# Optimization experiments

Hardware: AMD Instinct MI355X
Metric: run time of the kernel (lower is better)

Reference implementation:

```python
import jax, jax.numpy as jnp
import numpy as np

ALPHA = 1.702
LIMIT = 7.0


def setup_inputs() -> dict:
    key = jax.random.key(0)
    ks = jax.random.split(key, 7)
    B, S, H, D, E, TOPK = 2, 2048, 2048, 2048, 8, 4
    T = B * S
    hidden_states = jax.random.normal(ks[0], (B, S, H), dtype=jnp.float32)
    gate_up_proj = jax.random.normal(ks[1], (E, H, 2 * D), dtype=jnp.float32) * 0.02
    gate_up_proj_bias = jax.random.normal(ks[2], (E, 2 * D), dtype=jnp.float32) * 0.02
    down_proj = jax.random.normal(ks[3], (E, D, H), dtype=jnp.float32) * 0.02
    down_proj_bias = jax.random.normal(ks[4], (E, H), dtype=jnp.float32) * 0.02
    rw = jax.random.uniform(ks[5], (T, E), dtype=jnp.float32)
    routing_weights = rw / jnp.sum(rw, axis=-1, keepdims=True)
    router_indices = jax.random.randint(ks[6], (T, TOPK), 0, E, dtype=jnp.int64)
    return {
        "hidden_states": hidden_states,
        "gate_up_proj": gate_up_proj,
        "gate_up_proj_bias": gate_up_proj_bias,
        "down_proj": down_proj,
        "down_proj_bias": down_proj_bias,
        "routing_weights": routing_weights,
        "router_indices": router_indices,
    }


def geglu(gate_up):
    # interleaved layout: gate = [..., 0::2], up = [..., 1::2]
    gate = gate_up[..., 0::2]
    up = gate_up[..., 1::2]
    gate = jnp.minimum(gate, LIMIT)
    up = jnp.clip(up, -LIMIT, LIMIT)
    glu = gate * jax.nn.sigmoid(gate * ALPHA)
    return (up + 1.0) * glu


def reference(hidden_states, gate_up_proj, gate_up_proj_bias, down_proj,
              down_proj_bias, routing_weights, router_indices):
    B, S, H = hidden_states.shape
    x = hidden_states.reshape(-1, H)  # [T, H]
    # per-expert batched GEMM: [E, T, 2D]
    gate_up = jnp.einsum('th,ehd->etd', x, gate_up_proj) + gate_up_proj_bias[:, None, :]
    act = geglu(gate_up)  # [E, T, D]
    out = jnp.einsum('etd,edh->eth', act, down_proj) + down_proj_bias[:, None, :]
    # weight by router probs and sum over experts
    out = out * routing_weights.T[:, :, None]  # [E, T, H]
    out = jnp.sum(out, axis=0)
    return out.reshape(B, S, H)
```

## Files before the change

kernel.cpp:

```cpp
#include <hip/hip_runtime.h>
#include <hip/hip_bf16.h>

#define ALPHA 1.702f
#define GLIMIT 7.0f

typedef __attribute__((ext_vector_type(4))) float f32x4;
typedef __attribute__((ext_vector_type(8))) __bf16 bf16x8;
typedef __attribute__((ext_vector_type(8))) short short8;

typedef __attribute__((address_space(3))) unsigned int as3_uint;
typedef const __attribute__((address_space(1))) unsigned int as1_uint;

__device__ __forceinline__ void async_copy16(void* lds, const void* g) {
    __builtin_amdgcn_global_load_lds((as1_uint*)g, (as3_uint*)lds, 16, 0, 0);
}

__device__ __forceinline__ short f2bf(float f) {
    unsigned u = __float_as_uint(f);
    unsigned r = (u + 0x7fffu + ((u >> 16) & 1u)) >> 16;
    return (short)r;
}

__global__ void cvt_bf16_kernel(const float* __restrict__ src,
                                short* __restrict__ dst, int n4) {
    int i = blockIdx.x * blockDim.x + threadIdx.x;
    if (i < n4) {
        float4 v = reinterpret_cast<const float4*>(src)[i];
        short4 o;
        o.x = f2bf(v.x); o.y = f2bf(v.y); o.z = f2bf(v.z); o.w = f2bf(v.w);
        reinterpret_cast<short4*>(dst)[i] = o;
    }
}

__global__ void transpose_cvt(const float* __restrict__ src,
                              short* __restrict__ dst, int R, int C) {
    __shared__ float t[64][65];
    const int z  = blockIdx.z;
    const int c0 = blockIdx.x * 64;
    const int r0 = blockIdx.y * 64;
    const float* s = src + (size_t)z * R * C;
    short* d = dst + (size_t)z * R * C;
    const int tid = threadIdx.x;
#pragma unroll
    for (int i = 0; i < 16; ++i) {
        int idx = i * 256 + tid;
        int r = idx >> 6, c = idx & 63;
        t[r][c] = s[(size_t)(r0 + r) * C + c0 + c];
    }
    __syncthreads();
#pragma unroll
    for (int i = 0; i < 16; ++i) {
        int idx = i * 256 + tid;
        int r = idx >> 6, c = idx & 63;
        d[(size_t)(c0 + r) * R + r0 + c] = f2bf(t[c][r]);
    }
}


struct Gemm1Src {
    const short* A; const short* B;
    __device__ __forceinline__ const short* operator()(int t, int h) const {
        const short* base = (h & 2) ? B : A;
        return base + ((size_t)(h & 1) << 18) + (size_t)t * 64;
    }
};

struct Gemm2Src {
    const short* act; const short* wdt; size_t aoff, boff; int kh;
    __device__ __forceinline__ const short* operator()(int t, int h) const {
        int g = (kh << 7) + t;
        int e = g >> 5;
        size_t ko = (size_t)(g & 31) << 6;
        if (h & 2) return wdt + ((size_t)e << 22) + boff + ((size_t)(h & 1) << 18) + ko;
        return act + ((size_t)e << 23) + aoff + ((size_t)(h & 1) << 18) + ko;
    }
};

#define PH_BAR()  __builtin_amdgcn_s_barrier()
#define PH_LGKM() do { asm volatile("s_waitcnt lgkmcnt(0)" ::: "memory"); \
                       __builtin_amdgcn_sched_barrier(0); } while (0)
#define VMW(n)    asm volatile("s_waitcnt vmcnt(" #n ")" ::: "memory")

template <typename Src>
__device__ __forceinline__ void gemm_8phase(const Src& src, int NT, char* smem,
                                            f32x4 (&acc)[8][4]) {
    const int tid  = threadIdx.x;
    const int lane = tid & 63;
    const int wid  = tid >> 6;
    const int wr   = wid >> 2;
    const int wcol = wid & 3;
    const int lhi  = lane >> 4;
    const int llo  = lane & 15;

    auto stage = [&](int buf, int h, const short* g) {
        char* dst = smem + buf * 65536 + h * 16384;
        {
            int c = tid, r = c >> 3, s = (c & 7) ^ (r & 7);
            async_copy16(dst + c * 16, g + (size_t)r * 2048 + s * 8);
        }
        {
            int c = tid + 512, r = c >> 3, s = (c & 7) ^ (r & 7);
            async_copy16(dst + c * 16, g + (size_t)r * 2048 + s * 8);
        }
    };
    auto ldfrag = [&](int buf, int h, int row, int slot) {
        return *(const bf16x8*)(smem + buf * 65536 + h * 16384 + row * 128 +
                                ((slot ^ (row & 7)) << 4));
    };

    stage(0, 0, src(0, 0)); stage(0, 2, src(0, 2));
    stage(0, 3, src(0, 3)); stage(0, 1, src(0, 1));
    stage(1, 0, src(1, 0)); stage(1, 2, src(1, 2)); stage(1, 3, src(1, 3));
    VMW(8);
    PH_BAR();

    bf16x8 a[4][2], b[4][2];
#pragma unroll
    for (int n = 0; n < 2; ++n) {
        int row = wcol * 32 + n * 16 + llo;
        b[n][0] = ldfrag(0, 2, row, lhi);
        b[n][1] = ldfrag(0, 2, row, 4 + lhi);
    }

    for (int t = 0; t < NT; ++t) {
        const int cur = t & 1, nxt = cur ^ 1;
#pragma unroll
        for (int m = 0; m < 4; ++m) {
            int row = wr * 64 + m * 16 + llo;
            a[m][0] = ldfrag(cur, 0, row, lhi);
            a[m][1] = ldfrag(cur, 0, row, 4 + lhi);
        }
        if (t + 1 < NT) stage(nxt, 1, src(t + 1, 1));
        PH_BAR(); PH_LGKM();
        __builtin_amdgcn_s_setprio(1);
#pragma unroll
        for (int m = 0; m < 4; ++m)
#pragma unroll
            for (int n = 0; n < 2; ++n)
#pragma unroll
                for (int ks = 0; ks < 2; ++ks)
                    acc[m][n] = __builtin_amdgcn_mfma_f32_16x16x32_bf16(
                        a[m][ks], b[n][ks], acc[m][n], 0, 0, 0);
        __builtin_amdgcn_s_setprio(0);
        PH_BAR();
#pragma unroll
        for (int n = 0; n < 2; ++n) {
            int row = wcol * 32 + n * 16 + llo;
            b[2 + n][0] = ldfrag(cur, 3, row, lhi);
            b[2 + n][1] = ldfrag(cur, 3, row, 4 + lhi);
        }
        if (t + 2 < NT) { stage(cur, 0, src(t + 2, 0)); VMW(10); }
        else if (t + 1 < NT) { VMW(8); }
        else { VMW(0); }
        PH_BAR(); PH_LGKM();
        __builtin_amdgcn_s_setprio(1);
#pragma unroll
        for (int m = 0; m < 4; ++m)
#pragma unroll
            for (int n = 2; n < 4; ++n)
#pragma unroll
                for (int ks = 0; ks < 2; ++ks)
                    acc[m][n] = __builtin_amdgcn_mfma_f32_16x16x32_bf16(
                        a[m][ks], b[n][ks], acc[m][n], 0, 0, 0);
        __builtin_amdgcn_s_setprio(0);
        PH_BAR();
#pragma unroll
        for (int m = 0; m < 4; ++m) {
            int row = wr * 64 + m * 16 + llo;
            a[m][0] = ldfrag(cur, 1, row, lhi);
            a[m][1] = ldfrag(cur, 1, row, 4 + lhi);
        }
        if (t + 2 < NT) stage(cur, 2, src(t + 2, 2));
        PH_BAR(); PH_LGKM();
        __builtin_amdgcn_s_setprio(1);
#pragma unroll
        for (int m = 0; m < 4; ++m)
#pragma unroll
            for (int n = 0; n < 2; ++n)
#pragma unroll
                for (int ks = 0; ks < 2; ++ks)
                    acc[4 + m][n] = __builtin_amdgcn_mfma_f32_16x16x32_bf16(
                        a[m][ks], b[n][ks], acc[4 + m][n], 0, 0, 0);
        __builtin_amdgcn_s_setprio(0);
        PH_BAR();
        if (t + 2 < NT) { stage(cur, 3, src(t + 2, 3)); VMW(8); }
        else if (t + 1 < NT) { VMW(2); }
        else { VMW(0); }
        PH_BAR(); PH_LGKM();
        __builtin_amdgcn_s_setprio(1);
        if (t + 1 < NT) {
#pragma unroll
            for (int n = 0; n < 2; ++n) {
                int row = wcol * 32 + n * 16 + llo;
                b[n][0] = ldfrag(nxt, 2, row, lhi);
                b[n][1] = ldfrag(nxt, 2, row, 4 + lhi);
            }
        }
#pragma unroll
        for (int m = 0; m < 4; ++m)
#pragma unroll
            for (int n = 2; n < 4; ++n)
#pragma unroll
                for (int ks = 0; ks < 2; ++ks)
                    acc[4 + m][n] = __builtin_amdgcn_mfma_f32_16x16x32_bf16(
                        a[m][ks], b[n][ks], acc[4 + m][n], 0, 0, 0);
        __builtin_amdgcn_s_setprio(0);
        PH_BAR();
    }
}

__global__ __launch_bounds__(512, 2) void gemm1_8ph(
    const short* __restrict__ xb, const short* __restrict__ wgut,
    const float* __restrict__ bias, const float* __restrict__ rwp,
    short* __restrict__ act) {
    __shared__ __align__(16) char smem[131072];
    const int e = blockIdx.z;
    int flat = blockIdx.x + (blockIdx.y << 4);
    int swz = (flat & 7) * 32 + (flat >> 3);
    const int n0 = (swz & 15) * 256;
    const int m0 = (swz >> 4) * 256;
    const int tid  = threadIdx.x;
    const int lane = tid & 63;
    const int wid  = tid >> 6;
    const int wr = wid >> 2, wcol = wid & 3;
    const int lhi = lane >> 4, llo = lane & 15;

    f32x4 acc[8][4];
#pragma unroll
    for (int m = 0; m < 8; ++m)
#pragma unroll
        for (int n = 0; n < 4; ++n) acc[m][n] = (f32x4){0.f, 0.f, 0.f, 0.f};

    Gemm1Src src{ xb + (size_t)m0 * 2048,
                  wgut + ((size_t)e << 23) + (size_t)n0 * 2048 };
    gemm_8phase(src, 32, smem, acc);

    short* lact = (short*)smem;
    float* rws  = (float*)(smem + 69632);
    if (tid < 256) rws[tid] = rwp[(size_t)(m0 + tid) * 8 + e];
    __syncthreads();

    const float* bias_e = bias + (size_t)e * 4096;
    const int par = lane & 1;
#pragma unroll
    for (int n = 0; n < 4; ++n) {
        int clocal = (n >> 1) * 128 + wcol * 32 + (n & 1) * 16 + llo;
        float bv = bias_e[n0 + clocal];
        int dloc = clocal >> 1;
#pragma unroll
        for (int m = 0; m < 8; ++m) {
            int rowb = (m >> 2) * 128 + wr * 64 + (m & 3) * 16 + (lhi << 2);
            float v[4], o[4];
#pragma unroll
            for (int j = 0; j < 4; ++j) v[j] = acc[m][n][j] + bv;
#pragma unroll
            for (int j = 0; j < 4; ++j) o[j] = __shfl_xor(v[j], 1);
#pragma unroll
            for (int jj = 0; jj < 2; ++jj) {
                int j = (par << 1) + jj;
                float g = par ? o[j] : v[j];
                float u = par ? v[j] : o[j];
                g = fminf(g, GLIMIT);
                u = fmaxf(fminf(u, GLIMIT), -GLIMIT);
                float glu = g / (1.f + __expf(-ALPHA * g));
                int row = rowb + j;
                lact[row * 136 + dloc] = f2bf((u + 1.f) * glu * rws[row]);
            }
        }
    }
    __syncthreads();
    short* acte = act + ((size_t)e << 23) + (size_t)m0 * 2048 + (n0 >> 1);
#pragma unroll
    for (int it = 0; it < 8; ++it) {
        int idx = it * 512 + tid;
        int row = idx >> 4, c8 = (idx & 15) << 3;
        *(short8*)(acte + (size_t)row * 2048 + c8) =
            *(const short8*)(lact + row * 136 + c8);
    }
}

__global__ __launch_bounds__(512, 2) void gemm2_8ph(
    const short* __restrict__ act, const short* __restrict__ wdt,
    float* __restrict__ out, float* __restrict__ part) {
    __shared__ __align__(16) char smem[131072];
    const int kh = blockIdx.z;
    int flat = blockIdx.x + (blockIdx.y << 3);
    int swz = (flat & 7) * 16 + (flat >> 3);
    const int n0 = (swz & 7) * 256;
    const int m0 = (swz >> 3) * 256;
    const int tid  = threadIdx.x;
    const int lane = tid & 63;
    const int wid  = tid >> 6;
    const int wr = wid >> 2, wcol = wid & 3;

    f32x4 acc[8][4];
#pragma unroll
    for (int m = 0; m < 8; ++m)
#pragma unroll
        for (int n = 0; n < 4; ++n) acc[m][n] = (f32x4){0.f, 0.f, 0.f, 0.f};

    Gemm2Src src{ act, wdt, (size_t)m0 * 2048, (size_t)n0 * 2048, kh };
    gemm_8phase(src, 128, smem, acc);

    float* dst = (kh == 0) ? out : part;
#pragma unroll
    for (int m = 0; m < 8; ++m) {
        int row = m0 + (m >> 2) * 128 + wr * 64 + (m & 3) * 16 + ((lane >> 4) << 2);
#pragma unroll
        for (int n = 0; n < 4; ++n) {
            int col = n0 + (n >> 1) * 128 + wcol * 32 + (n & 1) * 16 + (lane & 15);
#pragma unroll
            for (int j = 0; j < 4; ++j)
                dst[(size_t)(row + j) * 2048 + col] = acc[m][n][j];
        }
    }
}

__global__ __launch_bounds__(256) void reduce_bias(
    const float* __restrict__ p1, const float* __restrict__ rw,
    const float* __restrict__ bd, float* __restrict__ out) {
    const int t = blockIdx.x;
    const int tid = threadIdx.x;
    float rwv[8];
#pragma unroll
    for (int e = 0; e < 8; ++e) rwv[e] = rw[(size_t)t * 8 + e];
    size_t base = (size_t)t * 2048;
#pragma unroll
    for (int i = 0; i < 2; ++i) {
        int h = (tid + i * 256) * 4;
        float4 o = *(const float4*)(out + base + h);
        float4 p = *(const float4*)(p1 + base + h);
        o.x += p.x; o.y += p.y; o.z += p.z; o.w += p.w;
#pragma unroll
        for (int e = 0; e < 8; ++e) {
            float4 bb = *(const float4*)(bd + e * 2048 + h);
            o.x += rwv[e] * bb.x; o.y += rwv[e] * bb.y;
            o.z += rwv[e] * bb.z; o.w += rwv[e] * bb.w;
        }
        *(float4*)(out + base + h) = o;
    }
}

extern "C" void kernel_launch(void* const* d_in, const int* in_sizes, int n_in,
                              void* d_out, int out_size, void* d_ws, size_t ws_size,
                              hipStream_t stream) {
    const float* x   = (const float*)d_in[0];
    const float* wgu = (const float*)d_in[1];
    const float* bgu = (const float*)d_in[2];
    const float* wd  = (const float*)d_in[3];
    const float* bd  = (const float*)d_in[4];
    const float* rw  = (const float*)d_in[5];
    float* out = (float*)d_out;

    char* ws = (char*)d_ws;
    short* xb   = (short*)(ws);
    short* wgut = (short*)(ws + 16777216);
    float* p1   = (float*)(ws + 16777216);
    short* wdt  = (short*)(ws + 150994944);
    short* actb = (short*)(ws + 218103808);

    cvt_bf16_kernel<<<8192, 256, 0, stream>>>(x, xb, 2097152);
    transpose_cvt<<<dim3(64, 32, 8), 256, 0, stream>>>(wgu, wgut, 2048, 4096);
    transpose_cvt<<<dim3(32, 32, 8), 256, 0, stream>>>(wd, wdt, 2048, 2048);
    gemm1_8ph<<<dim3(16, 16, 8), 512, 0, stream>>>(xb, wgut, bgu, rw, actb);
    gemm2_8ph<<<dim3(8, 16, 2), 512, 0, stream>>>(actb, wdt, out, p1);
    reduce_bias<<<4096, 256, 0, stream>>>(p1, rw, bd, out);
}
```

Measured before the change: 964.1 us.

## Make gemm1 persistent over experts with in-loop fused GEGLU epilogue

The first GEMM now runs one workgroup per output tile that loops over all 8 experts in a single 256-step k-loop, instead of launching a separate workgroup per expert. After every 32 steps an epilogue lambda applies bias, GEGLU and the routing weight and writes bf16 activations straight to global memory, while the next expert's tiles are already being prefetched. Tile placement is remapped so each XCD handles a fixed set of weight columns, aiming for better L2 reuse of the shared input rows and the weights, and bias/routing weights are staged in LDS once up front. The trade-off is scattered 2-byte global stores in place of the earlier LDS-staged, vectorized writeback, plus extra LDS use for the staging buffers.

Measured after the change: 1.093 ms. 13.4% more time.

```diff
diff --git a/kernel.cpp b/kernel.cpp
--- a/kernel.cpp
+++ b/kernel.cpp
@@ -57,11 +57,13 @@
 }
 
 
-struct Gemm1Src {
+struct Gemm1PSrc {
     const short* A; const short* B;
     __device__ __forceinline__ const short* operator()(int t, int h) const {
-        const short* base = (h & 2) ? B : A;
-        return base + ((size_t)(h & 1) << 18) + (size_t)t * 64;
+        int e = t >> 5;
+        size_t ko = (size_t)(t & 31) << 6;
+        if (h & 2) return B + ((size_t)e << 23) + ((size_t)(h & 1) << 18) + ko;
+        return A + ((size_t)(h & 1) << 18) + ko;
     }
 };
 
@@ -81,9 +83,9 @@
                        __builtin_amdgcn_sched_barrier(0); } while (0)
 #define VMW(n)    asm volatile("s_waitcnt vmcnt(" #n ")" ::: "memory")
 
-template <typename Src>
-__device__ __forceinline__ void gemm_8phase(const Src& src, int NT, char* smem,
-                                            f32x4 (&acc)[8][4]) {
+template <int NT, int SEG, typename Src, typename Epi>
+__device__ __forceinline__ void gemm_8phase(const Src& src, char* smem,
+                                            f32x4 (&acc)[8][4], const Epi& epi) {
     const int tid  = threadIdx.x;
     const int lane = tid & 63;
     const int wid  = tid >> 6;
@@ -206,6 +208,17 @@
                         a[m][ks], b[n][ks], acc[4 + m][n], 0, 0, 0);
         __builtin_amdgcn_s_setprio(0);
         PH_BAR();
+        if (((t + 1) & (SEG - 1)) == 0) {
+            epi(t / SEG, acc);
+            if (t + 1 < NT) {
+                VMW(8);
+#pragma unroll
+                for (int m = 0; m < 8; ++m)
+#pragma unroll
+                    for (int n = 0; n < 4; ++n)
+                        acc[m][n] = (f32x4){0.f, 0.f, 0.f, 0.f};
+            }
+        }
     }
 }
 
@@ -214,69 +227,66 @@
     const float* __restrict__ bias, const float* __restrict__ rwp,
     short* __restrict__ act) {
     __shared__ __align__(16) char smem[131072];
-    const int e = blockIdx.z;
-    int flat = blockIdx.x + (blockIdx.y << 4);
-    int swz = (flat & 7) * 32 + (flat >> 3);
-    const int n0 = (swz & 15) * 256;
-    const int m0 = (swz >> 4) * 256;
+    __shared__ float rws2[2048];
+    __shared__ float bias2[2048];
+    const int bid = blockIdx.x;
+    const int xcd = bid & 7, j = bid >> 3;
+    const int n0 = (((xcd << 1) + (j >> 4)) << 8);
+    const int m0 = ((j & 15) << 8);
     const int tid  = threadIdx.x;
     const int lane = tid & 63;
     const int wid  = tid >> 6;
     const int wr = wid >> 2, wcol = wid & 3;
     const int lhi = lane >> 4, llo = lane & 15;
 
+    ((float4*)rws2)[tid] = ((const float4*)(rwp + (size_t)m0 * 8))[tid];
+    {
+        int idx = tid << 2;
+        int ei = idx >> 8, c = idx & 255;
+        ((float4*)bias2)[tid] =
+            *(const float4*)(bias + (size_t)ei * 4096 + n0 + c);
+    }
+
     f32x4 acc[8][4];
 #pragma unroll
     for (int m = 0; m < 8; ++m)
 #pragma unroll
         for (int n = 0; n < 4; ++n) acc[m][n] = (f32x4){0.f, 0.f, 0.f, 0.f};
 
-    Gemm1Src src{ xb + (size_t)m0 * 2048,
-                  wgut + ((size_t)e << 23) + (size_t)n0 * 2048 };
-    gemm_8phase(src, 32, smem, acc);
-
-    short* lact = (short*)smem;
-    float* rws  = (float*)(smem + 69632);
-    if (tid < 256) rws[tid] = rwp[(size_t)(m0 + tid) * 8 + e];
-    __syncthreads();
-
-    const float* bias_e = bias + (size_t)e * 4096;
+    Gemm1PSrc src{ xb + (size_t)m0 * 2048, wgut + (size_t)n0 * 2048 };
     const int par = lane & 1;
-#pragma unroll
-    for (int n = 0; n < 4; ++n) {
-        int clocal = (n >> 1) * 128 + wcol * 32 + (n & 1) * 16 + llo;
-        float bv = bias_e[n0 + clocal];
-        int dloc = clocal >> 1;
-#pragma unroll
-        for (int m = 0; m < 8; ++m) {
-            int rowb = (m >> 2) * 128 + wr * 64 + (m & 3) * 16 + (lhi << 2);
-            float v[4], o[4];
-#pragma unroll
-            for (int j = 0; j < 4; ++j) v[j] = acc[m][n][j] + bv;
-#pragma unroll
-            for (int j = 0; j < 4; ++j) o[j] = __shfl_xor(v[j], 1);
-#pragma unroll
-            for (int jj = 0; jj < 2; ++jj) {
-                int j = (par << 1) + jj;
-                float g = par ? o[j] : v[j];
-                float u = par ? v[j] : o[j];
-                g = fminf(g, GLIMIT);
-                u = fmaxf(fminf(u, GLIMIT), -GLIMIT);
-                float glu = g / (1.f + __expf(-ALPHA * g));
-                int row = rowb + j;
-                lact[row * 136 + dloc] = f2bf((u + 1.f) * glu * rws[row]);
+
+    auto epi = [&](int e, f32x4 (&ac)[8][4]) {
+        short* acte = act + ((size_t)e << 23);
+#pragma unroll
+        for (int n = 0; n < 4; ++n) {
+            int clocal = (n >> 1) * 128 + wcol * 32 + (n & 1) * 16 + llo;
+            float bv = bias2[(e << 8) + clocal];
+            int dcol = (n0 + clocal) >> 1;
+#pragma unroll
+            for (int m = 0; m < 8; ++m) {
+                int rowb = (m >> 2) * 128 + wr * 64 + (m & 3) * 16 + (lhi << 2);
+                float v[4], o[4];
+#pragma unroll
+                for (int q = 0; q < 4; ++q) v[q] = ac[m][n][q] + bv;
+#pragma unroll
+                for (int q = 0; q < 4; ++q) o[q] = __shfl_xor(v[q], 1);
+#pragma unroll
+                for (int jj = 0; jj < 2; ++jj) {
+                    int q = (par << 1) + jj;
+                    float g = par ? o[q] : v[q];
+                    float u = par ? v[q] : o[q];
+                    g = fminf(g, GLIMIT);
+                    u = fmaxf(fminf(u, GLIMIT), -GLIMIT);
+                    float glu = g / (1.f + __expf(-ALPHA * g));
+                    int row = rowb + q;
+                    float aa = (u + 1.f) * glu * rws2[row * 8 + e];
+                    acte[(size_t)(m0 + row) * 2048 + dcol] = f2bf(aa);
+                }
             }
         }
-    }
-    __syncthreads();
-    short* acte = act + ((size_t)e << 23) + (size_t)m0 * 2048 + (n0 >> 1);
-#pragma unroll
-    for (int it = 0; it < 8; ++it) {
-        int idx = it * 512 + tid;
-        int row = idx >> 4, c8 = (idx & 15) << 3;
-        *(short8*)(acte + (size_t)row * 2048 + c8) =
-            *(const short8*)(lact + row * 136 + c8);
-    }
+    };
+    gemm_8phase<256, 32>(src, smem, acc, epi);
 }
 
 __global__ __launch_bounds__(512, 2) void gemm2_8ph(
@@ -300,20 +310,22 @@
         for (int n = 0; n < 4; ++n) acc[m][n] = (f32x4){0.f, 0.f, 0.f, 0.f};
 
     Gemm2Src src{ act, wdt, (size_t)m0 * 2048, (size_t)n0 * 2048, kh };
-    gemm_8phase(src, 128, smem, acc);
-
     float* dst = (kh == 0) ? out : part;
-#pragma unroll
-    for (int m = 0; m < 8; ++m) {
-        int row = m0 + (m >> 2) * 128 + wr * 64 + (m & 3) * 16 + ((lane >> 4) << 2);
-#pragma unroll
-        for (int n = 0; n < 4; ++n) {
-            int col = n0 + (n >> 1) * 128 + wcol * 32 + (n & 1) * 16 + (lane & 15);
-#pragma unroll
-            for (int j = 0; j < 4; ++j)
-                dst[(size_t)(row + j) * 2048 + col] = acc[m][n][j];
-        }
-    }
+
+    auto epi = [&](int, f32x4 (&ac)[8][4]) {
+#pragma unroll
+        for (int m = 0; m < 8; ++m) {
+            int row = m0 + (m >> 2) * 128 + wr * 64 + (m & 3) * 16 + ((lane >> 4) << 2);
+#pragma unroll
+            for (int n = 0; n < 4; ++n) {
+                int col = n0 + (n >> 1) * 128 + wcol * 32 + (n & 1) * 16 + (lane & 15);
+#pragma unroll
+                for (int q = 0; q < 4; ++q)
+                    dst[(size_t)(row + q) * 2048 + col] = ac[m][n][q];
+            }
+        }
+    };
+    gemm_8phase<128, 128>(src, smem, acc, epi);
 }
 
 __global__ __launch_bounds__(256) void reduce_bias(
@@ -362,7 +374,7 @@
     cvt_bf16_kernel<<<8192, 256, 0, stream>>>(x, xb, 2097152);
     transpose_cvt<<<dim3(64, 32, 8), 256, 0, stream>>>(wgu, wgut, 2048, 4096);
     transpose_cvt<<<dim3(32, 32, 8), 256, 0, stream>>>(wd, wdt, 2048, 2048);
-    gemm1_8ph<<<dim3(16, 16, 8), 512, 0, stream>>>(xb, wgut, bgu, rw, actb);
+    gemm1_8ph<<<256, 512, 0, stream>>>(xb, wgut, bgu, rw, actb);
     gemm2_8ph<<<dim3(8, 16, 2), 512, 0, stream>>>(actb, wdt, out, p1);
     reduce_bias<<<4096, 256, 0, stream>>>(p1, rw, bd, out);
 }
```
